# Kernel tuning notes

Hardware: AMD Instinct MI355X
Metric: run time of the kernel (lower is better)

Reference implementation:

```python
import jax, jax.numpy as jnp
import numpy as np

D_MODEL = 512
N_HEADS = 8
HEAD_DIM = D_MODEL // N_HEADS
D_FF = 2048
EPS = 1e-5


def layer_norm(x, gamma, beta):
    mu = jnp.mean(x, axis=-1, keepdims=True)
    var = jnp.mean((x - mu) ** 2, axis=-1, keepdims=True)
    return (x - mu) * jax.lax.rsqrt(var + EPS) * gamma + beta


def setup_inputs() -> dict:
    key = jax.random.key(0)
    ks = jax.random.split(key, 17)
    B, S = 2, 2048
    s_in = 1.0 / np.sqrt(D_MODEL)
    s_ff = 1.0 / np.sqrt(D_FF)
    return {
        "x": jax.random.normal(ks[0], (B, S, D_MODEL), jnp.float32),
        "Wq": jax.random.normal(ks[1], (D_MODEL, D_MODEL), jnp.float32) * s_in,
        "bq": jnp.zeros((D_MODEL,), jnp.float32),
        "Wk": jax.random.normal(ks[2], (D_MODEL, D_MODEL), jnp.float32) * s_in,
        "bk": jnp.zeros((D_MODEL,), jnp.float32),
        "Wv": jax.random.normal(ks[3], (D_MODEL, D_MODEL), jnp.float32) * s_in,
        "bv": jnp.zeros((D_MODEL,), jnp.float32),
        "Wo": jax.random.normal(ks[4], (D_MODEL, D_MODEL), jnp.float32) * s_in,
        "bo": jnp.zeros((D_MODEL,), jnp.float32),
        "W1": jax.random.normal(ks[5], (D_MODEL, D_FF), jnp.float32) * s_in,
        "b1": jnp.zeros((D_FF,), jnp.float32),
        "W2": jax.random.normal(ks[6], (D_FF, D_MODEL), jnp.float32) * s_ff,
        "b2": jnp.zeros((D_MODEL,), jnp.float32),
        "g1": jnp.ones((D_MODEL,), jnp.float32),
        "be1": jnp.zeros((D_MODEL,), jnp.float32),
        "g2": jnp.ones((D_MODEL,), jnp.float32),
        "be2": jnp.zeros((D_MODEL,), jnp.float32),
    }


def reference(x, Wq, bq, Wk, bk, Wv, bv, Wo, bo, W1, b1, W2, b2, g1, be1, g2, be2):
    B, S, _ = x.shape
    # projections + split heads -> [B, H, S, Dh]
    def heads(t):
        return t.reshape(B, S, N_HEADS, HEAD_DIM).transpose(0, 2, 1, 3)
    q = heads(x @ Wq + bq)
    k = heads(x @ Wk + bk)
    v = heads(x @ Wv + bv)
    # explicit scaled dot-product attention (full [B,H,S,S] scores as in source)
    scores = jnp.einsum('bhqd,bhkd->bhqk', q, k) / np.sqrt(HEAD_DIM).astype(np.float32)
    attn = jax.nn.softmax(scores, axis=-1)
    ctx = jnp.einsum('bhqk,bhkd->bhqd', attn, v)
    ctx = ctx.transpose(0, 2, 1, 3).reshape(B, S, D_MODEL)
    attn_out = ctx @ Wo + bo
    # post-norm residual 1
    h = layer_norm(x + attn_out, g1, be1)
    # FFN
    ff = jax.nn.relu(h @ W1 + b1) @ W2 + b2
    # post-norm residual 2
    return layer_norm(h + ff, g2, be2)
```

## Files before the change

### kernel.cpp

```cpp
#include <hip/hip_runtime.h>
#include <cmath>

#define D_MODEL 512
#define N_HEADS 8
#define HEAD_DIM 64
#define D_FF 2048
#define SEQ 2048
#define BATCH 2
#define MROWS (BATCH * SEQ)

typedef __attribute__((ext_vector_type(8))) short short8;
typedef __attribute__((ext_vector_type(4))) float float4v;
typedef unsigned short ushort_t;

static __device__ __forceinline__ ushort_t f2bf(float f) {
    union { float f; unsigned u; } v; v.f = f;
    unsigned r = (v.u + 0x7FFFu + ((v.u >> 16) & 1u)) >> 16;
    return (ushort_t)r;
}
static __device__ __forceinline__ ushort_t f2bf_trunc(float f) {
    union { float f; unsigned u; } v; v.f = f;
    return (ushort_t)(v.u >> 16);
}
static __device__ __forceinline__ float bf2f(ushort_t b) {
    union { unsigned u; float f; } v; v.u = ((unsigned)b) << 16;
    return v.f;
}

static __device__ __forceinline__ void gload16(const void* g, void* l) {
    __builtin_amdgcn_global_load_lds(
        (__attribute__((address_space(1))) void*)(unsigned long long)g,
        (__attribute__((address_space(3))) void*)(unsigned)(unsigned long long)l,
        16, 0, 0);
}

__global__ __launch_bounds__(256) void prep_k(
    const float* __restrict__ x,
    const float* __restrict__ Wq, const float* __restrict__ Wk,
    const float* __restrict__ Wv, const float* __restrict__ Wo,
    const float* __restrict__ W1, const float* __restrict__ W2,
    ushort_t* __restrict__ xb,
    ushort_t* __restrict__ WqkvT, ushort_t* __restrict__ WoT,
    ushort_t* __restrict__ W1T, ushort_t* __restrict__ W2T)
{
    int tile = blockIdx.x;
    if (tile >= 3072) {
        int i = (tile - 3072) * 256 + threadIdx.x;
        float4 f = ((const float4*)x)[i];
        ushort4 o;
        o.x = f2bf(f.x); o.y = f2bf(f.y); o.z = f2bf(f.z); o.w = f2bf(f.w);
        ((ushort4*)xb)[i] = o;
        return;
    }
    const float* src; ushort_t* dst; int Kd, Nd, tloc;
    if (tile < 1024) {
        int wsel = tile >> 8; tloc = tile & 255; Kd = 512; Nd = 512;
        if (wsel == 0)      { src = Wq; dst = WqkvT; }
        else if (wsel == 1) { src = Wk; dst = WqkvT + (size_t)512 * 512; }
        else if (wsel == 2) { src = Wv; dst = WqkvT + (size_t)1024 * 512; }
        else                { src = Wo; dst = WoT; }
    } else if (tile < 2048) { tloc = tile - 1024; Kd = 512;  Nd = 2048; src = W1; dst = W1T; }
    else                    { tloc = tile - 2048; Kd = 2048; Nd = 512;  src = W2; dst = W2T; }
    int tn = Nd >> 5;
    int k0 = (tloc / tn) << 5, n0 = (tloc % tn) << 5;
    __shared__ float tl[32][33];
    int c = threadIdx.x & 31, r = threadIdx.x >> 5;
    #pragma unroll
    for (int i = 0; i < 4; ++i)
        tl[r + i * 8][c] = src[(size_t)(k0 + r + i * 8) * Nd + n0 + c];
    __syncthreads();
    #pragma unroll
    for (int i = 0; i < 4; ++i)
        dst[(size_t)(n0 + r + i * 8) * Kd + k0 + c] = f2bf(tl[c][r + i * 8]);
}

template <int MODE>
__global__ __launch_bounds__(256) void gemm_std_k(
    const ushort_t* __restrict__ A, const ushort_t* __restrict__ BT,
    const float* __restrict__ bias, void* __restrict__ Cv,
    int N, int K, int Klen, size_t zstride)
{
    __shared__ ushort_t As[64 * 128];
    __shared__ ushort_t Bs[128 * 128];

    const int t = threadIdx.x;
    const int w = t >> 6, lane = t & 63, l16 = lane & 15, quad = lane >> 4;
    const int m0 = blockIdx.y * 64;
    const int n0 = blockIdx.x * 128;
    const int kbase = blockIdx.z * Klen;
    const int mbase = (w >> 1) * 32;
    const int nbase = (w & 1) * 64;
    const int lrow = lane >> 4;
    const int lchunk = lane & 15;

    float4v acc[2][4];
    #pragma unroll
    for (int mt = 0; mt < 2; ++mt)
        #pragma unroll
        for (int nt = 0; nt < 4; ++nt)
            acc[mt][nt] = (float4v){0.f, 0.f, 0.f, 0.f};

    for (int ks = kbase; ks < kbase + Klen; ks += 128) {
        __syncthreads();
        for (int c = w; c < 16; c += 4) {
            int rl = c * 4 + lrow;
            gload16(A + (size_t)(m0 + rl) * K + ks + ((lchunk ^ (rl & 7)) << 3),
                    &As[c * 512]);
        }
        for (int c = w; c < 32; c += 4) {
            int rl = c * 4 + lrow;
            gload16(BT + (size_t)(n0 + rl) * K + ks + ((lchunk ^ (rl & 7)) << 3),
                    &Bs[c * 512]);
        }
        __syncthreads();

        #pragma unroll
        for (int co = 0; co < 4; ++co) {
            const int poff = (((co * 4 + quad) ^ (l16 & 7)) << 3);
            short8 af[2], bf8[4];
            #pragma unroll
            for (int mt = 0; mt < 2; ++mt)
                af[mt] = *(const short8*)&As[(mbase + mt * 16 + l16) * 128 + poff];
            #pragma unroll
            for (int nt = 0; nt < 4; ++nt)
                bf8[nt] = *(const short8*)&Bs[(nbase + nt * 16 + l16) * 128 + poff];
            #pragma unroll
            for (int mt = 0; mt < 2; ++mt)
                #pragma unroll
                for (int nt = 0; nt < 4; ++nt)
                    acc[mt][nt] = __builtin_amdgcn_mfma_f32_16x16x32_bf16(
                        af[mt], bf8[nt], acc[mt][nt], 0, 0, 0);
        }
    }

    float* Cf = (float*)Cv + blockIdx.z * zstride;
    #pragma unroll
    for (int mt = 0; mt < 2; ++mt) {
        #pragma unroll
        for (int nt = 0; nt < 4; ++nt) {
            int gcol = n0 + nbase + nt * 16 + l16;
            float b = (MODE == 2) ? 0.f : bias[gcol];
            #pragma unroll
            for (int r = 0; r < 4; ++r) {
                int grow = m0 + mbase + mt * 16 + quad * 4 + r;
                float v = acc[mt][nt][r] + b;
                if (MODE == 1) v = fmaxf(v, 0.f);
                if (MODE == 1) ((ushort_t*)Cv)[(size_t)grow * N + gcol] = f2bf(v);
                else           Cf[(size_t)grow * N + gcol] = v;
            }
        }
    }
}

__global__ __launch_bounds__(256) void gemm_qkv_k(
    const ushort_t* __restrict__ A, const ushort_t* __restrict__ BT,
    const float* __restrict__ bq, const float* __restrict__ bk,
    const float* __restrict__ bv,
    ushort_t* __restrict__ Qb, ushort_t* __restrict__ Kb,
    ushort_t* __restrict__ VTb)
{
    __shared__ ushort_t As[64 * 128];
    __shared__ ushort_t Bs[128 * 128];

    const int t = threadIdx.x;
    const int w = t >> 6, lane = t & 63, l16 = lane & 15, quad = lane >> 4;
    const int m0 = blockIdx.y * 64;
    const int n0 = blockIdx.x * 128;
    const int mbase = (w >> 1) * 32;
    const int nbase = (w & 1) * 64;
    const int lrow = lane >> 4;
    const int lchunk = lane & 15;
    const int K = 512;

    float4v acc[2][4];
    #pragma unroll
    for (int mt = 0; mt < 2; ++mt)
        #pragma unroll
        for (int nt = 0; nt < 4; ++nt)
            acc[mt][nt] = (float4v){0.f, 0.f, 0.f, 0.f};

    for (int ks = 0; ks < 512; ks += 128) {
        __syncthreads();
        for (int c = w; c < 16; c += 4) {
            int rl = c * 4 + lrow;
            gload16(A + (size_t)(m0 + rl) * K + ks + ((lchunk ^ (rl & 7)) << 3),
                    &As[c * 512]);
        }
        for (int c = w; c < 32; c += 4) {
            int rl = c * 4 + lrow;
            gload16(BT + (size_t)(n0 + rl) * K + ks + ((lchunk ^ (rl & 7)) << 3),
                    &Bs[c * 512]);
        }
        __syncthreads();

        #pragma unroll
        for (int co = 0; co < 4; ++co) {
            const int poff = (((co * 4 + quad) ^ (l16 & 7)) << 3);
            short8 af[2], bf8[4];
            #pragma unroll
            for (int mt = 0; mt < 2; ++mt)
                af[mt] = *(const short8*)&As[(mbase + mt * 16 + l16) * 128 + poff];
            #pragma unroll
            for (int nt = 0; nt < 4; ++nt)
                bf8[nt] = *(const short8*)&Bs[(nbase + nt * 16 + l16) * 128 + poff];
            #pragma unroll
            for (int mt = 0; mt < 2; ++mt)
                #pragma unroll
                for (int nt = 0; nt < 4; ++nt)
                    acc[mt][nt] = __builtin_amdgcn_mfma_f32_16x16x32_bf16(
                        af[mt], bf8[nt], acc[mt][nt], 0, 0, 0);
        }
    }

    const int tsel = n0 >> 9;
    const float* bias = (tsel == 0) ? bq : (tsel == 1) ? bk : bv;
    const float scl = (tsel == 0) ? 0.18033688f : 1.0f;
    ushort_t* dst = (tsel == 0) ? Qb : Kb;

    #pragma unroll
    for (int mt = 0; mt < 2; ++mt) {
        #pragma unroll
        for (int nt = 0; nt < 4; ++nt) {
            int gcol = n0 + nbase + nt * 16 + l16;
            int lcol = gcol - (tsel << 9);
            int h = lcol >> 6, dh = lcol & 63;
            float b = bias[lcol];
            #pragma unroll
            for (int r = 0; r < 4; ++r) {
                int grow = m0 + mbase + mt * 16 + quad * 4 + r;
                int bb = grow >> 11, s = grow & 2047;
                float v = (acc[mt][nt][r] + b) * scl;
                if (tsel < 2)
                    dst[(((size_t)(bb * N_HEADS + h)) * SEQ + s) * HEAD_DIM + dh] = f2bf(v);
                else
                    VTb[(((size_t)(bb * N_HEADS + h)) * HEAD_DIM + dh) * SEQ + s] = f2bf(v);
            }
        }
    }
}

__global__ __launch_bounds__(256) void attn_mfma_k(
    const ushort_t* __restrict__ Qg, const ushort_t* __restrict__ Kg,
    const ushort_t* __restrict__ VTg,
    ushort_t* __restrict__ Ctx)
{
    __shared__ __align__(16) ushort_t Kbuf[2][128 * 64];
    __shared__ __align__(16) ushort_t Vbuf[2][64 * 128];

    const int bh = blockIdx.x;
    const int q0 = blockIdx.y * 64;
    const int t = threadIdx.x;
    const int w = t >> 6;
    const int lane = t & 63;
    const int l16 = lane & 15;
    const int quad = lane >> 4;
    const int qbase = q0 + w * 16;
    const float NM2 = -14.4269504f;

    const int rA = t >> 3;
    const int gk = (t & 7) ^ (rA & 7);
    const int kpA = (rA & 3) | ((rA & 0x0C) << 1) | ((rA & 0x10) >> 2);
    const int rv = t >> 4;
    const int gv = (t & 15) ^ (rv & 7);
    const size_t kgrow = (size_t)bh * SEQ;
    const size_t vgrow = (size_t)bh * HEAD_DIM;

#define ATTN_STAGE(b, kb)                                                                   \
    {                                                                                       \
        gload16(Kg + (kgrow + (kb) + kpA)      * HEAD_DIM + gk * 8, &Kbuf[b][w * 512]);     \
        gload16(Kg + (kgrow + (kb) + kpA + 32) * HEAD_DIM + gk * 8, &Kbuf[b][2048 + w * 512]); \
        gload16(Kg + (kgrow + (kb) + kpA + 64) * HEAD_DIM + gk * 8, &Kbuf[b][4096 + w * 512]); \
        gload16(Kg + (kgrow + (kb) + kpA + 96) * HEAD_DIM + gk * 8, &Kbuf[b][6144 + w * 512]); \
        gload16(VTg + (vgrow + rv)      * SEQ + (kb) + gv * 8, &Vbuf[b][w * 512]);          \
        gload16(VTg + (vgrow + rv + 16) * SEQ + (kb) + gv * 8, &Vbuf[b][2048 + w * 512]);   \
        gload16(VTg + (vgrow + rv + 32) * SEQ + (kb) + gv * 8, &Vbuf[b][4096 + w * 512]);   \
        gload16(VTg + (vgrow + rv + 48) * SEQ + (kb) + gv * 8, &Vbuf[b][6144 + w * 512]);   \
    }

    short8 aq[2];
    {
        const ushort_t* qp = Qg + ((size_t)bh * SEQ + qbase + l16) * HEAD_DIM + quad * 8;
        aq[0] = *(const short8*)(qp);
        aq[1] = *(const short8*)(qp + 32);
    }

    const short8 ones8 = {(short)0x3F80, (short)0x3F80, (short)0x3F80, (short)0x3F80,
                          (short)0x3F80, (short)0x3F80, (short)0x3F80, (short)0x3F80};

    float4v o[4] = {};
    float4v ol = {};

    ATTN_STAGE(0, 0)

    for (int i = 0; i < 16; ++i) {
        const int cur = i & 1;
        if (i < 15) {
            ATTN_STAGE(cur ^ 1, (i + 1) * 128)
            asm volatile("s_waitcnt vmcnt(8) lgkmcnt(0)" ::: "memory");
        } else {
            asm volatile("s_waitcnt vmcnt(0) lgkmcnt(0)" ::: "memory");
        }
        asm volatile("s_barrier" ::: "memory");

        const ushort_t* Kc = Kbuf[cur];
        const ushort_t* Vc = Vbuf[cur];

        float4v s[8];
        #pragma unroll
        for (int nt = 0; nt < 8; ++nt)
            s[nt] = (float4v){NM2, NM2, NM2, NM2};

        __builtin_amdgcn_s_setprio(1);
        #pragma unroll
        for (int c = 0; c < 2; ++c) {
            const int poff = (((c * 4 + quad) ^ (l16 & 7)) << 3);
            #pragma unroll
            for (int nt = 0; nt < 8; ++nt) {
                short8 bk8 = *(const short8*)&Kc[(nt * 16 + l16) * 64 + poff];
                s[nt] = __builtin_amdgcn_mfma_f32_16x16x32_bf16(bk8, aq[c], s[nt], 0, 0, 0);
            }
        }
        __builtin_amdgcn_s_setprio(0);

        #pragma unroll
        for (int nt = 0; nt < 8; ++nt)
            #pragma unroll
            for (int r = 0; r < 4; ++r)
                s[nt][r] = exp2f(s[nt][r]);

        __builtin_amdgcn_s_setprio(1);
        #pragma unroll
        for (int c = 0; c < 4; ++c) {
            short8 af;
            af[0] = (short)f2bf_trunc(s[2 * c][0]);
            af[1] = (short)f2bf_trunc(s[2 * c][1]);
            af[2] = (short)f2bf_trunc(s[2 * c][2]);
            af[3] = (short)f2bf_trunc(s[2 * c][3]);
            af[4] = (short)f2bf_trunc(s[2 * c + 1][0]);
            af[5] = (short)f2bf_trunc(s[2 * c + 1][1]);
            af[6] = (short)f2bf_trunc(s[2 * c + 1][2]);
            af[7] = (short)f2bf_trunc(s[2 * c + 1][3]);
            const int poff = (((c * 4 + quad) ^ (l16 & 7)) << 3);
            #pragma unroll
            for (int dt = 0; dt < 4; ++dt) {
                short8 bv8 = *(const short8*)&Vc[(dt * 16 + l16) * 128 + poff];
                o[dt] = __builtin_amdgcn_mfma_f32_16x16x32_bf16(af, bv8, o[dt], 0, 0, 0);
            }
            ol = __builtin_amdgcn_mfma_f32_16x16x32_bf16(af, ones8, ol, 0, 0, 0);
        }
        __builtin_amdgcn_s_setprio(0);

        asm volatile("s_barrier" ::: "memory");
    }
#undef ATTN_STAGE

    const int bb = bh >> 3, hh = bh & 7;
    #pragma unroll
    for (int r = 0; r < 4; ++r) {
        int q = qbase + quad * 4 + r;
        float inv = 1.0f / ol[r];
        #pragma unroll
        for (int dt = 0; dt < 4; ++dt)
            Ctx[((size_t)(bb * SEQ + q)) * D_MODEL + hh * HEAD_DIM + dt * 16 + l16] =
                f2bf(o[dt][r] * inv);
    }
}

__global__ __launch_bounds__(256) void wo_ln_k(
    const ushort_t* __restrict__ Ctx,
    const ushort_t* __restrict__ WoT,
    const float* __restrict__ x,
    const float* __restrict__ bo,
    const float* __restrict__ gam, const float* __restrict__ bet,
    ushort_t* __restrict__ Hhb)
{
    __shared__ __align__(16) ushort_t As[16 * 512];
    __shared__ __align__(16) ushort_t Bs[2][512 * 64];
    __shared__ float red[2][4][16];

    const int t = threadIdx.x;
    const int w = t >> 6, lane = t & 63, l16 = lane & 15, quad = lane >> 4;
    const int m0 = blockIdx.x * 16;
    const int K = 512;

    #pragma unroll
    for (int p = 0; p < 4; ++p) {
        int row = p * 4 + w;
        int g = (lane & 56) | ((lane & 7) ^ (row & 7));
        gload16(Ctx + (size_t)(m0 + row) * K + g * 8, &As[row * 512]);
    }

#define WOLN_STAGE_B(b, ks)                                                     \
    {                                                                           \
        _Pragma("unroll")                                                       \
        for (int c = 0; c < 16; ++c) {                                          \
            int row = c * 32 + (t >> 3);                                        \
            int g = (t & 7) ^ (row & 7);                                        \
            gload16(WoT + (size_t)row * K + (ks) * 64 + g * 8,                  \
                    &Bs[b][c * 2048 + w * 512]);                                \
        }                                                                       \
    }

    float4v acc[8];
    #pragma unroll
    for (int nt = 0; nt < 8; ++nt) acc[nt] = (float4v){0.f, 0.f, 0.f, 0.f};

    WOLN_STAGE_B(0, 0)

    for (int ks = 0; ks < 8; ++ks) {
        const int cur = ks & 1;
        if (ks < 7) {
            WOLN_STAGE_B(cur ^ 1, ks + 1)
            asm volatile("s_waitcnt vmcnt(16) lgkmcnt(0)" ::: "memory");
        } else {
            asm volatile("s_waitcnt vmcnt(0) lgkmcnt(0)" ::: "memory");
        }
        asm volatile("s_barrier" ::: "memory");

        #pragma unroll
        for (int c = 0; c < 2; ++c) {
            const int poff = (((c * 4 + quad) ^ (l16 & 7)) << 3);
            short8 af = *(const short8*)&As[l16 * 512 + ks * 64 + poff];
            #pragma unroll
            for (int nt = 0; nt < 8; ++nt) {
                short8 bv = *(const short8*)&Bs[cur][(w * 128 + nt * 16 + l16) * 64 + poff];
                acc[nt] = __builtin_amdgcn_mfma_f32_16x16x32_bf16(af, bv, acc[nt], 0, 0, 0);
            }
        }
        asm volatile("s_barrier" ::: "memory");
    }
#undef WOLN_STAGE_B

    float v[8][4];
    float s[4] = {0.f, 0.f, 0.f, 0.f}, ss[4] = {0.f, 0.f, 0.f, 0.f};
    #pragma unroll
    for (int nt = 0; nt < 8; ++nt) {
        int col = w * 128 + nt * 16 + l16;
        float b = bo[col];
        #pragma unroll
        for (int r = 0; r < 4; ++r) {
            int grow = m0 + quad * 4 + r;
            float val = acc[nt][r] + b + x[(size_t)grow * D_MODEL + col];
            v[nt][r] = val;
            s[r] += val;
            ss[r] += val * val;
        }
    }
    #pragma unroll
    for (int r = 0; r < 4; ++r) {
        #pragma unroll
        for (int m = 1; m < 16; m <<= 1) {
            s[r]  += __shfl_xor(s[r], m);
            ss[r] += __shfl_xor(ss[r], m);
        }
    }
    if (l16 == 0) {
        #pragma unroll
        for (int r = 0; r < 4; ++r) {
            red[0][w][quad * 4 + r] = s[r];
            red[1][w][quad * 4 + r] = ss[r];
        }
    }
    __syncthreads();
    #pragma unroll
    for (int r = 0; r < 4; ++r) {
        int lrow = quad * 4 + r;
        float S  = red[0][0][lrow] + red[0][1][lrow] + red[0][2][lrow] + red[0][3][lrow];
        float SS = red[1][0][lrow] + red[1][1][lrow] + red[1][2][lrow] + red[1][3][lrow];
        float mu  = S * (1.0f / D_MODEL);
        float var = SS * (1.0f / D_MODEL) - mu * mu;
        float inv = rsqrtf(var + 1e-5f);
        int grow = m0 + lrow;
        #pragma unroll
        for (int nt = 0; nt < 8; ++nt) {
            int col = w * 128 + nt * 16 + l16;
            float o = (v[nt][r] - mu) * inv * gam[col] + bet[col];
            Hhb[(size_t)grow * D_MODEL + col] = f2bf(o);
        }
    }
}

__global__ __launch_bounds__(256) void add_ln_k(
    const ushort_t* __restrict__ Xb, const float* __restrict__ P0,
    const float* __restrict__ P1, const float* __restrict__ bias,
    const float* __restrict__ gam, const float* __restrict__ bet,
    float* __restrict__ O)
{
    const int row = blockIdx.x;
    const int t = threadIdx.x;
    const size_t ro = (size_t)row * D_MODEL;
    const int c0 = 2 * t;

    ushort2 xb2 = *(const ushort2*)&Xb[ro + c0];
    float2 p0 = *(const float2*)&P0[ro + c0];
    float2 p1 = *(const float2*)&P1[ro + c0];
    float2 bi = *(const float2*)&bias[c0];
    float v0 = bf2f(xb2.x) + p0.x + p1.x + bi.x;
    float v1 = bf2f(xb2.y) + p0.y + p1.y + bi.y;
    float s = v0 + v1;
    float ss = v0 * v0 + v1 * v1;
    #pragma unroll
    for (int off = 32; off > 0; off >>= 1) {
        s  += __shfl_down(s, off);
        ss += __shfl_down(ss, off);
    }
    __shared__ float sb[4], ssb[4];
    if ((t & 63) == 0) { sb[t >> 6] = s; ssb[t >> 6] = ss; }
    __syncthreads();
    float S  = sb[0] + sb[1] + sb[2] + sb[3];
    float SS = ssb[0] + ssb[1] + ssb[2] + ssb[3];
    float mu  = S * (1.0f / D_MODEL);
    float var = SS * (1.0f / D_MODEL) - mu * mu;
    float inv = rsqrtf(var + 1e-5f);
    float2 gm = *(const float2*)&gam[c0];
    float2 bt2 = *(const float2*)&bet[c0];
    float2 o2;
    o2.x = (v0 - mu) * inv * gm.x + bt2.x;
    o2.y = (v1 - mu) * inv * gm.y + bt2.y;
    *(float2*)&O[ro + c0] = o2;
}

extern "C" void kernel_launch(void* const* d_in, const int* in_sizes, int n_in,
                              void* d_out, int out_size, void* d_ws, size_t ws_size,
                              hipStream_t stream)
{
    const float* x   = (const float*)d_in[0];
    const float* Wq  = (const float*)d_in[1];
    const float* bq  = (const float*)d_in[2];
    const float* Wk  = (const float*)d_in[3];
    const float* bk  = (const float*)d_in[4];
    const float* Wv  = (const float*)d_in[5];
    const float* bv  = (const float*)d_in[6];
    const float* Wo  = (const float*)d_in[7];
    const float* bo  = (const float*)d_in[8];
    const float* W1  = (const float*)d_in[9];
    const float* b1  = (const float*)d_in[10];
    const float* W2  = (const float*)d_in[11];
    const float* b2  = (const float*)d_in[12];
    const float* g1  = (const float*)d_in[13];
    const float* be1 = (const float*)d_in[14];
    const float* g2  = (const float*)d_in[15];
    const float* be2 = (const float*)d_in[16];
    float* out = (float*)d_out;
    float* ws  = (float*)d_ws;

    ushort_t* WoT   = (ushort_t*)(ws);
    ushort_t* W1T   = (ushort_t*)(ws + 131072);
    ushort_t* W2T   = (ushort_t*)(ws + 655360);
    ushort_t* WqkvT = (ushort_t*)(ws + 1179648);
    ushort_t* xb    = (ushort_t*)(ws + 1572864);
    ushort_t* Qb    = (ushort_t*)(ws + 2621440);
    ushort_t* Kb    = (ushort_t*)(ws + 3670016);
    ushort_t* VTb   = (ushort_t*)(ws + 4718592);
    ushort_t* Ctx   = (ushort_t*)(ws + 5767168);
    float*    P0    = ws + 8978432;
    float*    P1    = ws + 11075584;
    ushort_t* FF1   = (ushort_t*)(ws + 1572864);
    ushort_t* Hhb   = (ushort_t*)(ws + 5767168);

    prep_k<<<5120, 256, 0, stream>>>(x, Wq, Wk, Wv, Wo, W1, W2, xb, WqkvT, WoT, W1T, W2T);

    gemm_qkv_k<<<dim3(12, 64), 256, 0, stream>>>(xb, WqkvT, bq, bk, bv, Qb, Kb, VTb);

    attn_mfma_k<<<dim3(16, 32), 256, 0, stream>>>(Qb, Kb, VTb, Ctx);

    wo_ln_k<<<256, 256, 0, stream>>>(Ctx, WoT, x, bo, g1, be1, Hhb);

    gemm_std_k<1><<<dim3(16, 64), 256, 0, stream>>>(
        Hhb, W1T, b1, FF1, 2048, 512, 512, 0);

    gemm_std_k<2><<<dim3(4, 64, 2), 256, 0, stream>>>(
        FF1, W2T, nullptr, P0, 512, 2048, 1024, (size_t)MROWS * D_MODEL);

    add_ln_k<<<4096, 256, 0, stream>>>(Hhb, P0, P1, b2, g2, be2, out);
}
```

Baseline: 201.2 us.

## Process two query tiles per wave in attention with half-size blocks

The attention kernel now runs 2 waves per block instead of 4, and each wave handles 32 query rows (two 16-row MFMA tiles) rather than 16. Each K and V fragment read from LDS feeds two MFMAs, which halves LDS read traffic per unit of compute. With half the threads, each thread issues twice as many global-to-LDS loads per stage, and the wait count is raised to match. The risks are higher register pressure from doubled accumulators and score tiles, less latency hiding per block, and more load-issue work per thread.

After: 210.6 us. +4.7%, slower.

```diff
diff --git a/kernel.cpp b/kernel.cpp
--- a/kernel.cpp
+++ b/kernel.cpp
@@ -239,7 +239,7 @@
     }
 }
 
-__global__ __launch_bounds__(256) void attn_mfma_k(
+__global__ __launch_bounds__(128) void attn_mfma_k(
     const ushort_t* __restrict__ Qg, const ushort_t* __restrict__ Kg,
     const ushort_t* __restrict__ VTg,
     ushort_t* __restrict__ Ctx)
@@ -254,41 +254,45 @@
     const int lane = t & 63;
     const int l16 = lane & 15;
     const int quad = lane >> 4;
-    const int qbase = q0 + w * 16;
+    const int qbase = q0 + w * 32;
     const float NM2 = -14.4269504f;
 
     const int rA = t >> 3;
     const int gk = (t & 7) ^ (rA & 7);
-    const int kpA = (rA & 3) | ((rA & 0x0C) << 1) | ((rA & 0x10) >> 2);
     const int rv = t >> 4;
     const int gv = (t & 15) ^ (rv & 7);
     const size_t kgrow = (size_t)bh * SEQ;
     const size_t vgrow = (size_t)bh * HEAD_DIM;
 
-#define ATTN_STAGE(b, kb)                                                                   \
-    {                                                                                       \
-        gload16(Kg + (kgrow + (kb) + kpA)      * HEAD_DIM + gk * 8, &Kbuf[b][w * 512]);     \
-        gload16(Kg + (kgrow + (kb) + kpA + 32) * HEAD_DIM + gk * 8, &Kbuf[b][2048 + w * 512]); \
-        gload16(Kg + (kgrow + (kb) + kpA + 64) * HEAD_DIM + gk * 8, &Kbuf[b][4096 + w * 512]); \
-        gload16(Kg + (kgrow + (kb) + kpA + 96) * HEAD_DIM + gk * 8, &Kbuf[b][6144 + w * 512]); \
-        gload16(VTg + (vgrow + rv)      * SEQ + (kb) + gv * 8, &Vbuf[b][w * 512]);          \
-        gload16(VTg + (vgrow + rv + 16) * SEQ + (kb) + gv * 8, &Vbuf[b][2048 + w * 512]);   \
-        gload16(VTg + (vgrow + rv + 32) * SEQ + (kb) + gv * 8, &Vbuf[b][4096 + w * 512]);   \
-        gload16(VTg + (vgrow + rv + 48) * SEQ + (kb) + gv * 8, &Vbuf[b][6144 + w * 512]);   \
-    }
-
-    short8 aq[2];
-    {
-        const ushort_t* qp = Qg + ((size_t)bh * SEQ + qbase + l16) * HEAD_DIM + quad * 8;
-        aq[0] = *(const short8*)(qp);
-        aq[1] = *(const short8*)(qp + 32);
+#define ATTN_STAGE(b, kb)                                                                     \
+    {                                                                                         \
+        _Pragma("unroll")                                                                     \
+        for (int c = 0; c < 8; ++c) {                                                         \
+            int kp = (c >> 1) * 32 + ((rA & 12) << 1) + ((c & 1) << 2) + (rA & 3);            \
+            gload16(Kg + (kgrow + (kb) + kp) * HEAD_DIM + gk * 8,                             \
+                    &Kbuf[b][c * 1024 + w * 512]);                                            \
+        }                                                                                     \
+        _Pragma("unroll")                                                                     \
+        for (int c = 0; c < 8; ++c) {                                                         \
+            gload16(VTg + (vgrow + c * 8 + rv) * SEQ + (kb) + gv * 8,                         \
+                    &Vbuf[b][c * 1024 + w * 512]);                                            \
+        }                                                                                     \
+    }
+
+    short8 aq[2][2];
+    #pragma unroll
+    for (int mt = 0; mt < 2; ++mt) {
+        const ushort_t* qp =
+            Qg + ((size_t)bh * SEQ + qbase + mt * 16 + l16) * HEAD_DIM + quad * 8;
+        aq[mt][0] = *(const short8*)(qp);
+        aq[mt][1] = *(const short8*)(qp + 32);
     }
 
     const short8 ones8 = {(short)0x3F80, (short)0x3F80, (short)0x3F80, (short)0x3F80,
                           (short)0x3F80, (short)0x3F80, (short)0x3F80, (short)0x3F80};
 
-    float4v o[4] = {};
-    float4v ol = {};
+    float4v o[2][4] = {};
+    float4v ol[2] = {};
 
     ATTN_STAGE(0, 0)
 
@@ -296,7 +300,7 @@
         const int cur = i & 1;
         if (i < 15) {
             ATTN_STAGE(cur ^ 1, (i + 1) * 128)
-            asm volatile("s_waitcnt vmcnt(8) lgkmcnt(0)" ::: "memory");
+            asm volatile("s_waitcnt vmcnt(16) lgkmcnt(0)" ::: "memory");
         } else {
             asm volatile("s_waitcnt vmcnt(0) lgkmcnt(0)" ::: "memory");
         }
@@ -305,10 +309,12 @@
         const ushort_t* Kc = Kbuf[cur];
         const ushort_t* Vc = Vbuf[cur];
 
-        float4v s[8];
-        #pragma unroll
-        for (int nt = 0; nt < 8; ++nt)
-            s[nt] = (float4v){NM2, NM2, NM2, NM2};
+        float4v s[2][8];
+        #pragma unroll
+        for (int mt = 0; mt < 2; ++mt)
+            #pragma unroll
+            for (int nt = 0; nt < 8; ++nt)
+                s[mt][nt] = (float4v){NM2, NM2, NM2, NM2};
 
         __builtin_amdgcn_s_setprio(1);
         #pragma unroll
@@ -317,36 +323,50 @@
             #pragma unroll
             for (int nt = 0; nt < 8; ++nt) {
                 short8 bk8 = *(const short8*)&Kc[(nt * 16 + l16) * 64 + poff];
-                s[nt] = __builtin_amdgcn_mfma_f32_16x16x32_bf16(bk8, aq[c], s[nt], 0, 0, 0);
+                #pragma unroll
+                for (int mt = 0; mt < 2; ++mt)
+                    s[mt][nt] = __builtin_amdgcn_mfma_f32_16x16x32_bf16(
+                        bk8, aq[mt][c], s[mt][nt], 0, 0, 0);
             }
         }
         __builtin_amdgcn_s_setprio(0);
 
         #pragma unroll
-        for (int nt = 0; nt < 8; ++nt)
-            #pragma unroll
-            for (int r = 0; r < 4; ++r)
-                s[nt][r] = exp2f(s[nt][r]);
+        for (int mt = 0; mt < 2; ++mt)
+            #pragma unroll
+            for (int nt = 0; nt < 8; ++nt)
+                #pragma unroll
+                for (int r = 0; r < 4; ++r)
+                    s[mt][nt][r] = exp2f(s[mt][nt][r]);
 
         __builtin_amdgcn_s_setprio(1);
         #pragma unroll
         for (int c = 0; c < 4; ++c) {
-            short8 af;
-            af[0] = (short)f2bf_trunc(s[2 * c][0]);
-            af[1] = (short)f2bf_trunc(s[2 * c][1]);
-            af[2] = (short)f2bf_trunc(s[2 * c][2]);
-            af[3] = (short)f2bf_trunc(s[2 * c][3]);
-            af[4] = (short)f2bf_trunc(s[2 * c + 1][0]);
-            af[5] = (short)f2bf_trunc(s[2 * c + 1][1]);
-            af[6] = (short)f2bf_trunc(s[2 * c + 1][2]);
-            af[7] = (short)f2bf_trunc(s[2 * c + 1][3]);
+            short8 af[2];
+            #pragma unroll
+            for (int mt = 0; mt < 2; ++mt) {
+                af[mt][0] = (short)f2bf_trunc(s[mt][2 * c][0]);
+                af[mt][1] = (short)f2bf_trunc(s[mt][2 * c][1]);
+                af[mt][2] = (short)f2bf_trunc(s[mt][2 * c][2]);
+                af[mt][3] = (short)f2bf_trunc(s[mt][2 * c][3]);
+                af[mt][4] = (short)f2bf_trunc(s[mt][2 * c + 1][0]);
+                af[mt][5] = (short)f2bf_trunc(s[mt][2 * c + 1][1]);
+                af[mt][6] = (short)f2bf_trunc(s[mt][2 * c + 1][2]);
+                af[mt][7] = (short)f2bf_trunc(s[mt][2 * c + 1][3]);
+            }
             const int poff = (((c * 4 + quad) ^ (l16 & 7)) << 3);
             #pragma unroll
             for (int dt = 0; dt < 4; ++dt) {
                 short8 bv8 = *(const short8*)&Vc[(dt * 16 + l16) * 128 + poff];
-                o[dt] = __builtin_amdgcn_mfma_f32_16x16x32_bf16(af, bv8, o[dt], 0, 0, 0);
+                #pragma unroll
+                for (int mt = 0; mt < 2; ++mt)
+                    o[mt][dt] = __builtin_amdgcn_mfma_f32_16x16x32_bf16(
+                        af[mt], bv8, o[mt][dt], 0, 0, 0);
             }
-            ol = __builtin_amdgcn_mfma_f32_16x16x32_bf16(af, ones8, ol, 0, 0, 0);
+            #pragma unroll
+            for (int mt = 0; mt < 2; ++mt)
+                ol[mt] = __builtin_amdgcn_mfma_f32_16x16x32_bf16(
+                    af[mt], ones8, ol[mt], 0, 0, 0);
         }
         __builtin_amdgcn_s_setprio(0);
 
@@ -356,13 +376,16 @@
 
     const int bb = bh >> 3, hh = bh & 7;
     #pragma unroll
-    for (int r = 0; r < 4; ++r) {
-        int q = qbase + quad * 4 + r;
-        float inv = 1.0f / ol[r];
-        #pragma unroll
-        for (int dt = 0; dt < 4; ++dt)
-            Ctx[((size_t)(bb * SEQ + q)) * D_MODEL + hh * HEAD_DIM + dt * 16 + l16] =
-                f2bf(o[dt][r] * inv);
+    for (int mt = 0; mt < 2; ++mt) {
+        #pragma unroll
+        for (int r = 0; r < 4; ++r) {
+            int q = qbase + mt * 16 + quad * 4 + r;
+            float inv = 1.0f / ol[mt][r];
+            #pragma unroll
+            for (int dt = 0; dt < 4; ++dt)
+                Ctx[((size_t)(bb * SEQ + q)) * D_MODEL + hh * HEAD_DIM + dt * 16 + l16] =
+                    f2bf(o[mt][dt][r] * inv);
+        }
     }
 }
 
@@ -562,7 +585,7 @@
 
     gemm_qkv_k<<<dim3(12, 64), 256, 0, stream>>>(xb, WqkvT, bq, bk, bv, Qb, Kb, VTb);
 
-    attn_mfma_k<<<dim3(16, 32), 256, 0, stream>>>(Qb, Kb, VTb, Ctx);
+    attn_mfma_k<<<dim3(16, 32), 128, 0, stream>>>(Qb, Kb, VTb, Ctx);
 
     wo_ln_k<<<256, 256, 0, stream>>>(Ctx, WoT, x, bo, g1, be1, Hhb);
 
```
